# Kernel optimization log

Hardware: AMD Instinct MI355X
Metric: run time of the kernel (lower is better)

The kernel has to match this reference:

```python
import jax, jax.numpy as jnp
import numpy as np

B, S, D, H = 4, 2048, 1024, 16
DK = D // H


def setup_inputs() -> dict:
    key = jax.random.key(0)
    ks = jax.random.split(key, 12)
    s = 1.0 / np.sqrt(D)
    inp = {
        "q": jax.random.normal(ks[0], (B, S, D), jnp.float32),
        "k": jax.random.normal(ks[1], (B, S, D), jnp.float32),
        "v": jax.random.normal(ks[2], (B, S, D), jnp.float32),
        # causal mask, broadcastable over batch and heads
        "mask": jnp.tril(jnp.ones((S, S), jnp.int32))[None, None, :, :],
        "Wq": jax.random.uniform(ks[3], (D, D), jnp.float32, -s, s),
        "bq": jax.random.uniform(ks[4], (D,), jnp.float32, -s, s),
        "Wk": jax.random.uniform(ks[5], (D, D), jnp.float32, -s, s),
        "bk": jax.random.uniform(ks[6], (D,), jnp.float32, -s, s),
        "Wv": jax.random.uniform(ks[7], (D, D), jnp.float32, -s, s),
        "bv": jax.random.uniform(ks[8], (D,), jnp.float32, -s, s),
        "Wo": jax.random.uniform(ks[9], (D, D), jnp.float32, -s, s),
        "bo": jax.random.uniform(ks[10], (D,), jnp.float32, -s, s),
    }
    return inp


def reference(q, k, v, mask, Wq, bq, Wk, bk, Wv, bv, Wo, bo):
    def split_heads(x):  # [B,S,D] -> [B,H,S,DK]
        return x.reshape(B, S, H, DK).transpose(0, 2, 1, 3)

    qh = split_heads(q @ Wq.T + bq)
    kh = split_heads(k @ Wk.T + bk)
    vh = split_heads(v @ Wv.T + bv)

    scores = jnp.einsum("bhqd,bhkd->bhqk", qh, kh) / jnp.sqrt(jnp.float32(DK))
    scores = jnp.where(mask == 0, jnp.float32(-1e9), scores)
    attn = jax.nn.softmax(scores, axis=-1)
    out = jnp.einsum("bhqk,bhkd->bhqd", attn, vh)
    out = out.transpose(0, 2, 1, 3).reshape(B, S, D)
    return out @ Wo.T + bo
```

## Files before the change

kernel.cpp:

```cpp
#include <hip/hip_runtime.h>
#include <cstdint>

#define Bb 4
#define Ss 2048
#define Dd 1024
#define Hh 16

typedef unsigned short u16;
typedef unsigned int u32;
typedef __attribute__((ext_vector_type(8))) short short8;
typedef __attribute__((ext_vector_type(8))) _Float16 half8;
typedef __attribute__((ext_vector_type(2))) __fp16 fp16x2;
typedef __attribute__((ext_vector_type(4))) float floatx4;
typedef __attribute__((ext_vector_type(16))) float floatx16;
typedef __attribute__((address_space(3))) u32 lds_u32;
typedef const __attribute__((address_space(1))) u32 glob_u32;

__device__ __forceinline__ u16 f2bf(float x) {
  union { float f; u32 u; } v; v.f = x;
  u32 r = v.u + 0x7fffu + ((v.u >> 16) & 1u);
  return (u16)(r >> 16);
}

__device__ __forceinline__ u32 pk2(float a, float b) {
  union { fp16x2 h; u32 u; } cv;
  cv.h = __builtin_amdgcn_cvt_pkrtz(a, b);
  return cv.u;
}

__device__ __forceinline__ fp16x2 asH2(u32 x) {
  union { u32 u; fp16x2 h; } c; c.u = x; return c.h;
}

__device__ __forceinline__ half8 h8_from(u32 a, u32 b, u32 c, u32 d) {
  union { u32 u[4]; half8 h; } t;
  t.u[0] = a; t.u[1] = b; t.u[2] = c; t.u[3] = d;
  return t.h;
}

__global__ __launch_bounds__(256) void cvt_many(
    const float* __restrict__ s0, const float* __restrict__ s1,
    const float* __restrict__ s2, const float* __restrict__ s3,
    const float* __restrict__ s4, const float* __restrict__ s5,
    const float* __restrict__ s6, u16* __restrict__ d0, u16* __restrict__ d1,
    u16* __restrict__ d2, u16* __restrict__ d3, u16* __restrict__ d4,
    u16* __restrict__ d5, u16* __restrict__ d6, int nA, int nW) {
  int z = blockIdx.y;
  const float* s = z == 0 ? s0 : z == 1 ? s1 : z == 2 ? s2
                   : z == 3 ? s3 : z == 4 ? s4 : z == 5 ? s5 : s6;
  u16* d = z == 0 ? d0 : z == 1 ? d1 : z == 2 ? d2
           : z == 3 ? d3 : z == 4 ? d4 : z == 5 ? d5 : d6;
  int n8 = z < 3 ? nA : nW;
  int i = blockIdx.x * 256 + threadIdx.x;
  if (i >= n8) return;
  const float4* sp = (const float4*)s;
  float4 a = sp[2 * i], b = sp[2 * i + 1];
  u32 w0 = (u32)f2bf(a.x) | ((u32)f2bf(a.y) << 16);
  u32 w1 = (u32)f2bf(a.z) | ((u32)f2bf(a.w) << 16);
  u32 w2 = (u32)f2bf(b.x) | ((u32)f2bf(b.y) << 16);
  u32 w3 = (u32)f2bf(b.z) | ((u32)f2bf(b.w) << 16);
  ((uint4*)d)[i] = make_uint4(w0, w1, w2, w3);
}

template <int MODE>
__device__ __forceinline__ void gemm_body(const u16* __restrict__ A,
                                          const u16* __restrict__ Bw,
                                          const float* __restrict__ bias,
                                          void* __restrict__ Cout, float scale,
                                          int vtrans) {
  __shared__ u16 As[128 * 64];
  __shared__ u16 Bs[128 * 64];
  int tid = threadIdx.x;
  int wave = tid >> 6, lane = tid & 63;
  int quad = lane >> 4, l16 = lane & 15;
  int m0 = blockIdx.x * 128, n0 = blockIdx.y * 128;
  int wr = (wave >> 1) * 64, wc = (wave & 1) * 64;
  int s7 = l16 & 7;
  int srow = wave * 8 + (lane >> 3);
  int gcol = (((lane & 7) ^ (lane >> 3)) << 3);

  floatx4 vzero = {0.f, 0.f, 0.f, 0.f};
  floatx4 acc[4][4];
#pragma unroll
  for (int i = 0; i < 4; ++i)
#pragma unroll
    for (int j = 0; j < 4; ++j) acc[i][j] = vzero;

  for (int kt = 0; kt < Dd; kt += 64) {
    __syncthreads();
#pragma unroll
    for (int c = 0; c < 4; ++c) {
      int r = c * 32 + srow;
      __builtin_amdgcn_global_load_lds(
          (glob_u32*)&A[(size_t)(m0 + r) * Dd + kt + gcol],
          (lds_u32*)&As[(c * 32 + wave * 8) * 64], 16, 0, 0);
      __builtin_amdgcn_global_load_lds(
          (glob_u32*)&Bw[(size_t)(n0 + r) * Dd + kt + gcol],
          (lds_u32*)&Bs[(c * 32 + wave * 8) * 64], 16, 0, 0);
    }
    __syncthreads();
#pragma unroll
    for (int kk = 0; kk < 2; ++kk) {
      short8 af[4], bf[4];
#pragma unroll
      for (int i = 0; i < 4; ++i)
        af[i] = *(const short8*)&As[(wr + i * 16 + l16) * 64 + (((quad + 4 * kk) ^ s7) << 3)];
#pragma unroll
      for (int j = 0; j < 4; ++j)
        bf[j] = *(const short8*)&Bs[(wc + j * 16 + l16) * 64 + (((quad + 4 * kk) ^ s7) << 3)];
#pragma unroll
      for (int i = 0; i < 4; ++i)
#pragma unroll
        for (int j = 0; j < 4; ++j)
          acc[i][j] = __builtin_amdgcn_mfma_f32_16x16x32_bf16(af[i], bf[j], acc[i][j], 0, 0, 0);
    }
  }

#pragma unroll
  for (int i = 0; i < 4; ++i) {
#pragma unroll
    for (int j = 0; j < 4; ++j) {
      int n = n0 + wc + j * 16 + l16;
      if (MODE == 0 && vtrans) {
        int h = n >> 6, dk = n & 63;
        int b = m0 >> 11;
        int sb = (m0 + wr + i * 16 + quad * 4) & (Ss - 1);
        union { _Float16 h4[4]; uint2 u2; } pv;
#pragma unroll
        for (int r = 0; r < 4; ++r)
          pv.h4[r] = (_Float16)((acc[i][j][r] + bias[n]) * scale);
        *(uint2*)&((_Float16*)Cout)[((size_t)(b * Hh + h) * 64 + dk) * Ss + sb] = pv.u2;
      } else {
#pragma unroll
        for (int r = 0; r < 4; ++r) {
          int m = m0 + wr + i * 16 + quad * 4 + r;
          float val = (acc[i][j][r] + bias[n]) * scale;
          if (MODE == 0) {
            int b = m >> 11, s = m & (Ss - 1);
            int h = n >> 6, dk = n & 63;
            ((u16*)Cout)[((((size_t)b * Hh + h) * Ss + s) << 6) + dk] = f2bf(val);
          } else {
            ((float*)Cout)[(size_t)m * Dd + n] = val;
          }
        }
      }
    }
  }
}

__global__ __launch_bounds__(256) void gemm_qkv(const u16* qb, const u16* kb, const u16* vb,
                                                const u16* Wq, const u16* Wk, const u16* Wv,
                                                const float* bq, const float* bk, const float* bv,
                                                u16* qo, u16* ko, _Float16* vT) {
  const float K1 = 0.18033688f;
  int z = blockIdx.z;
  const u16* A = z == 0 ? qb : z == 1 ? kb : vb;
  const u16* W = z == 0 ? Wq : z == 1 ? Wk : Wv;
  const float* bi = z == 0 ? bq : z == 1 ? bk : bv;
  void* o = z == 0 ? (void*)qo : z == 1 ? (void*)ko : (void*)vT;
  gemm_body<0>(A, W, bi, o, z == 0 ? K1 : 1.0f, z == 2);
}

__global__ __launch_bounds__(256) void gemm_out(const u16* A, const u16* W,
                                                const float* bi, float* o) {
  gemm_body<1>(A, W, bi, o, 1.0f, 0);
}

#define MFIX 4.0f
#define SW(a, b) asm("v_permlane32_swap_b32 %0, %1" : "+v"(a), "+v"(b))
#define VRD(CH, NT) \
  (*(const half8*)&Vt[p][((NT) * 32 + l31) * 64 + ((((CH) + hi) ^ s7b) << 3)])

#define TILE_BODY(NST, MASKED)                                                \
  do {                                                                        \
    short8 kf0[4], kf1[4];                                                    \
    _Pragma("unroll") for (int m = 0; m < 4; ++m) {                           \
      kf0[m] = *(const short8*)&Kt[p][l31 * 64 + (((2 * m + hi) ^ s7b) << 3)];\
      if (NST == 2)                                                           \
        kf1[m] = *(const short8*)&Kt[p][(32 + l31) * 64 +                     \
                                        (((2 * m + hi) ^ s7b) << 3)];         \
    }                                                                         \
    floatx16 sc0, sc1;                                                        \
    __builtin_amdgcn_s_setprio(1);                                            \
    sc0 = __builtin_amdgcn_mfma_f32_32x32x16_bf16(kf0[0], qf[0], minit, 0, 0, 0); \
    if (NST == 2)                                                             \
      sc1 = __builtin_amdgcn_mfma_f32_32x32x16_bf16(kf1[0], qf[0], minit, 0, 0, 0); \
    _Pragma("unroll") for (int m = 1; m < 4; ++m) {                           \
      sc0 = __builtin_amdgcn_mfma_f32_32x32x16_bf16(kf0[m], qf[m], sc0, 0, 0, 0); \
      if (NST == 2)                                                           \
        sc1 = __builtin_amdgcn_mfma_f32_32x32x16_bf16(kf1[m], qf[m], sc1, 0, 0, 0); \
    }                                                                         \
    __builtin_amdgcn_s_setprio(0);                                            \
    if (MASKED) {                                                             \
      int qrow = Rq + l31;                                                    \
      _Pragma("unroll") for (int r = 0; r < 16; ++r) {                        \
        int key = k0 + 4 * hi + (r & 3) + 8 * (r >> 2);                       \
        if (key > qrow) sc0[r] = -3e38f;                                      \
        if (NST == 2 && key + 32 > qrow) sc1[r] = -3e38f;                     \
      }                                                                       \
    }                                                                         \
    u32 c0[8], c1[8];                                                         \
    _Pragma("unroll") for (int j = 0; j < 8; ++j) {                           \
      c0[j] = pk2(__builtin_amdgcn_exp2f(sc0[2 * j]),                         \
                  __builtin_amdgcn_exp2f(sc0[2 * j + 1]));                    \
      if (NST == 2)                                                           \
        c1[j] = pk2(__builtin_amdgcn_exp2f(sc1[2 * j]),                       \
                    __builtin_amdgcn_exp2f(sc1[2 * j + 1]));                  \
    }                                                                         \
    {                                                                         \
      fp16x2 t0 = asH2(c0[0]) + asH2(c0[1]);                                  \
      fp16x2 t1 = asH2(c0[2]) + asH2(c0[3]);                                  \
      fp16x2 t2 = asH2(c0[4]) + asH2(c0[5]);                                  \
      fp16x2 t3 = asH2(c0[6]) + asH2(c0[7]);                                  \
      fp16x2 ts = (t0 + t1) + (t2 + t3);                                      \
      if (NST == 2) {                                                         \
        fp16x2 u0 = asH2(c1[0]) + asH2(c1[1]);                                \
        fp16x2 u1 = asH2(c1[2]) + asH2(c1[3]);                                \
        fp16x2 u2 = asH2(c1[4]) + asH2(c1[5]);                                \
        fp16x2 u3 = asH2(c1[6]) + asH2(c1[7]);                                \
        ts = ts + ((u0 + u1) + (u2 + u3));                                    \
      }                                                                       \
      l_part += (float)ts[0] + (float)ts[1];                                  \
    }                                                                         \
    SW(c0[0], c0[2]); SW(c0[1], c0[3]); SW(c0[4], c0[6]); SW(c0[5], c0[7]);   \
    if (NST == 2) {                                                           \
      SW(c1[0], c1[2]); SW(c1[1], c1[3]); SW(c1[4], c1[6]); SW(c1[5], c1[7]); \
    }                                                                         \
    __builtin_amdgcn_s_setprio(1);                                            \
    {                                                                         \
      half8 pa = h8_from(c0[0], c0[1], c0[2], c0[3]);                         \
      o0a = __builtin_amdgcn_mfma_f32_32x32x16_f16(pa, VRD(0, 0), o0a, 0, 0, 0); \
      o1a = __builtin_amdgcn_mfma_f32_32x32x16_f16(pa, VRD(0, 1), o1a, 0, 0, 0); \
      half8 pb = h8_from(c0[4], c0[5], c0[6], c0[7]);                         \
      o0a = __builtin_amdgcn_mfma_f32_32x32x16_f16(pb, VRD(2, 0), o0a, 0, 0, 0); \
      o1a = __builtin_amdgcn_mfma_f32_32x32x16_f16(pb, VRD(2, 1), o1a, 0, 0, 0); \
      if (NST == 2) {                                                         \
        half8 pc = h8_from(c1[0], c1[1], c1[2], c1[3]);                       \
        o0b = __builtin_amdgcn_mfma_f32_32x32x16_f16(pc, VRD(4, 0), o0b, 0, 0, 0); \
        o1b = __builtin_amdgcn_mfma_f32_32x32x16_f16(pc, VRD(4, 1), o1b, 0, 0, 0); \
        half8 pd = h8_from(c1[4], c1[5], c1[6], c1[7]);                       \
        o0b = __builtin_amdgcn_mfma_f32_32x32x16_f16(pd, VRD(6, 0), o0b, 0, 0, 0); \
        o1b = __builtin_amdgcn_mfma_f32_32x32x16_f16(pd, VRD(6, 1), o1b, 0, 0, 0); \
      }                                                                       \
    }                                                                         \
    __builtin_amdgcn_s_setprio(0);                                            \
  } while (0)

__global__ __launch_bounds__(128) void attn_kernel(const u16* __restrict__ qh,
                                                   const u16* __restrict__ kh,
                                                   const _Float16* __restrict__ vT,
                                                   u16* __restrict__ ctx) {
  __shared__ u16 Kt[2][64 * 64];
  __shared__ _Float16 Vt[2][64 * 64];

  int tid = threadIdx.x, w = tid >> 6, lane = tid & 63;
  int hi = lane >> 5, l31 = lane & 31, s7b = lane & 7;
  int bh = blockIdx.x;
  int s = 31 - blockIdx.y;
  const u16* Q = qh + (size_t)bh * Ss * 64;
  const u16* K = kh + (size_t)bh * Ss * 64;
  const _Float16* V = vT + (size_t)bh * 64 * Ss;

  int Rq = 64 * s + 32 * w;

  short8 qf[4];
#pragma unroll
  for (int m = 0; m < 4; ++m)
    qf[m] = *(const short8*)&Q[(size_t)(Rq + l31) * 64 + m * 16 + hi * 8];

  floatx16 minit;
#pragma unroll
  for (int r = 0; r < 16; ++r) minit[r] = -MFIX;
  floatx16 o0a, o0b, o1a, o1b;
#pragma unroll
  for (int r = 0; r < 16; ++r) { o0a[r] = 0.f; o0b[r] = 0.f; o1a[r] = 0.f; o1b[r] = 0.f; }
  float l_part = 0.f;

  int srow = tid >> 3;
  int g8 = ((tid & 7) ^ ((tid >> 3) & 7)) << 3;

#define STAGE(P, KT)                                                          \
  do {                                                                        \
    int _k0 = (KT) * 64;                                                      \
    _Pragma("unroll") for (int c = 0; c < 4; ++c) {                           \
      int r_ = c * 16 + srow;                                                 \
      __builtin_amdgcn_global_load_lds(                                       \
          (glob_u32*)&K[(size_t)(_k0 + r_) * 64 + g8],                        \
          (lds_u32*)&Kt[P][(c * 16 + w * 8) * 64], 16, 0, 0);                 \
      __builtin_amdgcn_global_load_lds(                                       \
          (glob_u32*)&V[(size_t)r_ * Ss + _k0 + g8],                          \
          (lds_u32*)&Vt[P][(c * 16 + w * 8) * 64], 16, 0, 0);                 \
    }                                                                         \
  } while (0)

  STAGE(0, 0);

  int p = 0;
  for (int kt = 0; kt <= s; ++kt) {
    int k0 = kt * 64;
    __syncthreads();
    if (kt < s) STAGE(p ^ 1, kt + 1);

    if (kt < s) {
      TILE_BODY(2, false);
    } else if (w == 0) {
      TILE_BODY(1, true);
    } else {
      TILE_BODY(2, true);
    }
    p ^= 1;
  }
#undef STAGE

  float l2 = l_part + __shfl_xor(l_part, 32, 64);
  float linv = 1.0f / l2;
  int b = bh >> 4, h = bh & 15;
#pragma unroll
  for (int r = 0; r < 16; ++r) {
    int qi = (r & 3) + 8 * (r >> 2) + 4 * hi;
    float li = __shfl(linv, qi, 64);
    size_t base = ((size_t)b * Ss + Rq + qi) * Dd + h * 64 + l31;
    ctx[base] = f2bf((o0a[r] + o0b[r]) * li);
    ctx[base + 32] = f2bf((o1a[r] + o1b[r]) * li);
  }
}

extern "C" void kernel_launch(void* const* d_in, const int* in_sizes, int n_in,
                              void* d_out, int out_size, void* d_ws, size_t ws_size,
                              hipStream_t stream) {
  const float* q = (const float*)d_in[0];
  const float* k = (const float*)d_in[1];
  const float* v = (const float*)d_in[2];
  const float* Wq = (const float*)d_in[4];
  const float* bq = (const float*)d_in[5];
  const float* Wk = (const float*)d_in[6];
  const float* bk = (const float*)d_in[7];
  const float* Wv = (const float*)d_in[8];
  const float* bv = (const float*)d_in[9];
  const float* Wo = (const float*)d_in[10];
  const float* bo = (const float*)d_in[11];

  char* ws = (char*)d_ws;
  const size_t MB = 1024 * 1024;
  u16* qb = (u16*)(ws + 0 * MB);
  u16* kb = (u16*)(ws + 16 * MB);
  u16* vb = (u16*)(ws + 32 * MB);
  u16* Wqb = (u16*)(ws + 48 * MB);
  u16* Wkb = (u16*)(ws + 50 * MB);
  u16* Wvb = (u16*)(ws + 52 * MB);
  u16* Wob = (u16*)(ws + 54 * MB);
  u16* qhp = (u16*)(ws + 56 * MB);
  u16* khp = (u16*)(ws + 72 * MB);
  _Float16* vhT = (_Float16*)(ws + 88 * MB);
  u16* ctx = qb;

  const int nA8 = (Bb * Ss * Dd) / 8;
  const int nW8 = (Dd * Dd) / 8;
  {
    dim3 g(nA8 / 256, 7);
    cvt_many<<<g, 256, 0, stream>>>(q, k, v, Wq, Wk, Wv, Wo,
                                    qb, kb, vb, Wqb, Wkb, Wvb, Wob, nA8, nW8);
  }
  {
    dim3 g((Bb * Ss) / 128, Dd / 128, 3);
    gemm_qkv<<<g, 256, 0, stream>>>(qb, kb, vb, Wqb, Wkb, Wvb, bq, bk, bv, qhp, khp, vhT);
  }
  {
    dim3 g(Bb * Hh, 32);
    attn_kernel<<<g, 128, 0, stream>>>(qhp, khp, vhT, ctx);
  }
  {
    dim3 g((Bb * Ss) / 128, Dd / 128);
    gemm_out<<<g, 256, 0, stream>>>(ctx, Wob, bo, (float*)d_out);
  }
}
```

Measured before the change: 326.9 us.

## Enlarge attention query tile to 128 rows with 4 waves; flatten cvt grid

The attention kernel now uses 256 threads (4 waves) per block, each covering 32 query rows of a 128-row tile. Each staged K/V tile is therefore shared by twice as many queries, halving K/V global traffic per query. Causal masking is now decided per wave from its row range, and the duplicate output accumulators are merged into single o0/o1 accumulators to free registers. The conversion kernel switches to a flat 1D grid so the small weight slices no longer launch mostly-idle blocks. Risks are more idle waves near the diagonal and a serial MFMA accumulation chain.

```diff
diff --git a/kernel.cpp b/kernel.cpp
--- a/kernel.cpp
+++ b/kernel.cpp
@@ -44,15 +44,22 @@
     const float* __restrict__ s4, const float* __restrict__ s5,
     const float* __restrict__ s6, u16* __restrict__ d0, u16* __restrict__ d1,
     u16* __restrict__ d2, u16* __restrict__ d3, u16* __restrict__ d4,
-    u16* __restrict__ d5, u16* __restrict__ d6, int nA, int nW) {
-  int z = blockIdx.y;
+    u16* __restrict__ d5, u16* __restrict__ d6, int nAB, int nWB) {
+  int bid = blockIdx.x;
+  int z, i0;
+  if (bid < 3 * nAB) {
+    z = bid / nAB;
+    i0 = bid % nAB;
+  } else {
+    int r = bid - 3 * nAB;
+    z = 3 + r / nWB;
+    i0 = r % nWB;
+  }
   const float* s = z == 0 ? s0 : z == 1 ? s1 : z == 2 ? s2
                    : z == 3 ? s3 : z == 4 ? s4 : z == 5 ? s5 : s6;
   u16* d = z == 0 ? d0 : z == 1 ? d1 : z == 2 ? d2
            : z == 3 ? d3 : z == 4 ? d4 : z == 5 ? d5 : d6;
-  int n8 = z < 3 ? nA : nW;
-  int i = blockIdx.x * 256 + threadIdx.x;
-  if (i >= n8) return;
+  int i = i0 * 256 + threadIdx.x;
   const float4* sp = (const float4*)s;
   float4 a = sp[2 * i], b = sp[2 * i + 1];
   u32 w0 = (u32)f2bf(a.x) | ((u32)f2bf(a.y) << 16);
@@ -229,24 +236,24 @@
     __builtin_amdgcn_s_setprio(1);                                            \
     {                                                                         \
       half8 pa = h8_from(c0[0], c0[1], c0[2], c0[3]);                         \
-      o0a = __builtin_amdgcn_mfma_f32_32x32x16_f16(pa, VRD(0, 0), o0a, 0, 0, 0); \
-      o1a = __builtin_amdgcn_mfma_f32_32x32x16_f16(pa, VRD(0, 1), o1a, 0, 0, 0); \
+      o0 = __builtin_amdgcn_mfma_f32_32x32x16_f16(pa, VRD(0, 0), o0, 0, 0, 0);\
+      o1 = __builtin_amdgcn_mfma_f32_32x32x16_f16(pa, VRD(0, 1), o1, 0, 0, 0);\
       half8 pb = h8_from(c0[4], c0[5], c0[6], c0[7]);                         \
-      o0a = __builtin_amdgcn_mfma_f32_32x32x16_f16(pb, VRD(2, 0), o0a, 0, 0, 0); \
-      o1a = __builtin_amdgcn_mfma_f32_32x32x16_f16(pb, VRD(2, 1), o1a, 0, 0, 0); \
+      o0 = __builtin_amdgcn_mfma_f32_32x32x16_f16(pb, VRD(2, 0), o0, 0, 0, 0);\
+      o1 = __builtin_amdgcn_mfma_f32_32x32x16_f16(pb, VRD(2, 1), o1, 0, 0, 0);\
       if (NST == 2) {                                                         \
         half8 pc = h8_from(c1[0], c1[1], c1[2], c1[3]);                       \
-        o0b = __builtin_amdgcn_mfma_f32_32x32x16_f16(pc, VRD(4, 0), o0b, 0, 0, 0); \
-        o1b = __builtin_amdgcn_mfma_f32_32x32x16_f16(pc, VRD(4, 1), o1b, 0, 0, 0); \
+        o0 = __builtin_amdgcn_mfma_f32_32x32x16_f16(pc, VRD(4, 0), o0, 0, 0, 0); \
+        o1 = __builtin_amdgcn_mfma_f32_32x32x16_f16(pc, VRD(4, 1), o1, 0, 0, 0); \
         half8 pd = h8_from(c1[4], c1[5], c1[6], c1[7]);                       \
-        o0b = __builtin_amdgcn_mfma_f32_32x32x16_f16(pd, VRD(6, 0), o0b, 0, 0, 0); \
-        o1b = __builtin_amdgcn_mfma_f32_32x32x16_f16(pd, VRD(6, 1), o1b, 0, 0, 0); \
+        o0 = __builtin_amdgcn_mfma_f32_32x32x16_f16(pd, VRD(6, 0), o0, 0, 0, 0); \
+        o1 = __builtin_amdgcn_mfma_f32_32x32x16_f16(pd, VRD(6, 1), o1, 0, 0, 0); \
       }                                                                       \
     }                                                                         \
     __builtin_amdgcn_s_setprio(0);                                            \
   } while (0)
 
-__global__ __launch_bounds__(128) void attn_kernel(const u16* __restrict__ qh,
+__global__ __launch_bounds__(256) void attn_kernel(const u16* __restrict__ qh,
                                                    const u16* __restrict__ kh,
                                                    const _Float16* __restrict__ vT,
                                                    u16* __restrict__ ctx) {
@@ -256,12 +263,12 @@
   int tid = threadIdx.x, w = tid >> 6, lane = tid & 63;
   int hi = lane >> 5, l31 = lane & 31, s7b = lane & 7;
   int bh = blockIdx.x;
-  int s = 31 - blockIdx.y;
+  int s = 15 - blockIdx.y;
   const u16* Q = qh + (size_t)bh * Ss * 64;
   const u16* K = kh + (size_t)bh * Ss * 64;
   const _Float16* V = vT + (size_t)bh * 64 * Ss;
 
-  int Rq = 64 * s + 32 * w;
+  int Rq = 128 * s + 32 * w;
 
   short8 qf[4];
 #pragma unroll
@@ -271,9 +278,9 @@
   floatx16 minit;
 #pragma unroll
   for (int r = 0; r < 16; ++r) minit[r] = -MFIX;
-  floatx16 o0a, o0b, o1a, o1b;
-#pragma unroll
-  for (int r = 0; r < 16; ++r) { o0a[r] = 0.f; o0b[r] = 0.f; o1a[r] = 0.f; o1b[r] = 0.f; }
+  floatx16 o0, o1;
+#pragma unroll
+  for (int r = 0; r < 16; ++r) { o0[r] = 0.f; o1[r] = 0.f; }
   float l_part = 0.f;
 
   int srow = tid >> 3;
@@ -282,31 +289,31 @@
 #define STAGE(P, KT)                                                          \
   do {                                                                        \
     int _k0 = (KT) * 64;                                                      \
-    _Pragma("unroll") for (int c = 0; c < 4; ++c) {                           \
-      int r_ = c * 16 + srow;                                                 \
+    _Pragma("unroll") for (int c = 0; c < 2; ++c) {                           \
+      int r_ = c * 32 + srow;                                                 \
       __builtin_amdgcn_global_load_lds(                                       \
           (glob_u32*)&K[(size_t)(_k0 + r_) * 64 + g8],                        \
-          (lds_u32*)&Kt[P][(c * 16 + w * 8) * 64], 16, 0, 0);                 \
+          (lds_u32*)&Kt[P][(c * 32 + w * 8) * 64], 16, 0, 0);                 \
       __builtin_amdgcn_global_load_lds(                                       \
           (glob_u32*)&V[(size_t)r_ * Ss + _k0 + g8],                          \
-          (lds_u32*)&Vt[P][(c * 16 + w * 8) * 64], 16, 0, 0);                 \
+          (lds_u32*)&Vt[P][(c * 32 + w * 8) * 64], 16, 0, 0);                 \
     }                                                                         \
   } while (0)
 
   STAGE(0, 0);
 
   int p = 0;
-  for (int kt = 0; kt <= s; ++kt) {
+  int nt = 2 * s + 2;
+  for (int kt = 0; kt < nt; ++kt) {
     int k0 = kt * 64;
     __syncthreads();
-    if (kt < s) STAGE(p ^ 1, kt + 1);
-
-    if (kt < s) {
+    if (kt + 1 < nt) STAGE(p ^ 1, kt + 1);
+
+    if (k0 + 63 <= Rq) {
       TILE_BODY(2, false);
-    } else if (w == 0) {
-      TILE_BODY(1, true);
-    } else {
-      TILE_BODY(2, true);
+    } else if (k0 <= Rq + 31) {
+      if (k0 + 32 <= Rq + 31) TILE_BODY(2, true);
+      else TILE_BODY(1, true);
     }
     p ^= 1;
   }
@@ -320,8 +327,8 @@
     int qi = (r & 3) + 8 * (r >> 2) + 4 * hi;
     float li = __shfl(linv, qi, 64);
     size_t base = ((size_t)b * Ss + Rq + qi) * Dd + h * 64 + l31;
-    ctx[base] = f2bf((o0a[r] + o0b[r]) * li);
-    ctx[base + 32] = f2bf((o1a[r] + o1b[r]) * li);
+    ctx[base] = f2bf(o0[r] * li);
+    ctx[base + 32] = f2bf(o1[r] * li);
   }
 }
 
@@ -354,20 +361,20 @@
   _Float16* vhT = (_Float16*)(ws + 88 * MB);
   u16* ctx = qb;
 
-  const int nA8 = (Bb * Ss * Dd) / 8;
-  const int nW8 = (Dd * Dd) / 8;
+  const int nAB = (Bb * Ss * Dd) / 8 / 256;
+  const int nWB = (Dd * Dd) / 8 / 256;
   {
-    dim3 g(nA8 / 256, 7);
+    dim3 g(3 * nAB + 4 * nWB);
     cvt_many<<<g, 256, 0, stream>>>(q, k, v, Wq, Wk, Wv, Wo,
-                                    qb, kb, vb, Wqb, Wkb, Wvb, Wob, nA8, nW8);
+                                    qb, kb, vb, Wqb, Wkb, Wvb, Wob, nAB, nWB);
   }
   {
     dim3 g((Bb * Ss) / 128, Dd / 128, 3);
     gemm_qkv<<<g, 256, 0, stream>>>(qb, kb, vb, Wqb, Wkb, Wvb, bq, bk, bv, qhp, khp, vhT);
   }
   {
-    dim3 g(Bb * Hh, 32);
-    attn_kernel<<<g, 128, 0, stream>>>(qhp, khp, vhT, ctx);
+    dim3 g(Bb * Hh, 16);
+    attn_kernel<<<g, 256, 0, stream>>>(qhp, khp, vhT, ctx);
   }
   {
     dim3 g((Bb * Ss) / 128, Dd / 128);
```

Result: faster. 307.6 us (-5.9%).
